# Kernel optimization log

Hardware: AMD Instinct MI355X
Metric: run time of the kernel (lower is better)

The kernel has to match this reference:

```python
import jax, jax.numpy as jnp
import numpy as np
from jax import lax

NPOINT, RADIUS, NSAMPLE, EPS = 2048, 0.1, 32, 1e-5


def setup_inputs() -> dict:
    key = jax.random.key(0)
    ks = jax.random.split(key, 8)
    B, N, D, CIN, COUT, DEPTH = 4, 8192, 29, 32, 64, 2
    return {
        "xyz": jax.random.uniform(ks[0], (B, 3, N), jnp.float32),
        "points": jax.random.normal(ks[1], (B, D, N), jnp.float32),
        "proj_w": jax.random.normal(ks[2], (COUT, CIN), jnp.float32) * 0.05,
        "proj_g": jnp.ones((COUT,), jnp.float32),
        "proj_b": jnp.zeros((COUT,), jnp.float32),
        "w1": jax.random.normal(ks[3], (DEPTH, COUT, COUT), jnp.float32) * 0.05,
        "g1": jnp.ones((DEPTH, COUT), jnp.float32),
        "b1": jnp.zeros((DEPTH, COUT), jnp.float32),
        "w2": jax.random.normal(ks[4], (DEPTH, COUT, COUT), jnp.float32) * 0.05,
        "g2": jnp.ones((DEPTH, COUT), jnp.float32),
        "b2": jnp.zeros((DEPTH, COUT), jnp.float32),
    }


def fps(xyz, npoint):
    # xyz: [B,N,3] -> idx [B,npoint]; deterministic start at index 0
    B, N, _ = xyz.shape
    def body(carry, _):
        dist, far = carry  # [B,N], [B]
        centroid = jnp.take_along_axis(xyz, far[:, None, None], axis=1)  # [B,1,3]
        d = jnp.sum((xyz - centroid) ** 2, -1)
        dist = jnp.minimum(dist, d)
        return (dist, jnp.argmax(dist, -1).astype(jnp.int32)), far
    init = (jnp.full((B, N), 1e10, xyz.dtype), jnp.zeros((B,), jnp.int32))
    _, idx = lax.scan(body, init, None, length=npoint)
    return jnp.transpose(idx)  # [B,npoint]


def ball_query(radius, nsample, xyz, new_xyz):
    # matches torch query_ball_point: invalid -> N, sort, take first nsample, backfill
    N = xyz.shape[1]
    sqr = (jnp.sum(new_xyz ** 2, -1)[:, :, None]
           + jnp.sum(xyz ** 2, -1)[:, None, :]
           - 2.0 * jnp.einsum("bsc,bnc->bsn", new_xyz, xyz))  # [B,S,N]
    cand = jnp.where(sqr <= radius * radius, jnp.arange(N, dtype=jnp.int32), jnp.int32(N))
    neg, _ = lax.top_k(-cand, nsample)
    idx = -neg  # nsample smallest indices, ascending
    first = idx[:, :, :1]
    return jnp.where(idx == N, first, idx)  # [B,S,K]


def gather_nb(p, idx):
    # p [B,N,C], idx [B,S,K] -> [B,S,K,C]
    return jax.vmap(lambda pb, ib: pb[ib])(p, idx)


def _conv(x, w):
    # 1x1 conv: w [O,C], x [B,C,K,S]
    return jnp.einsum("oc,bcks->boks", w, x)


def _bn(x, g, b):
    # training-mode BatchNorm2d over (B,K,S) per channel
    m = jnp.mean(x, (0, 2, 3), keepdims=True)
    v = jnp.var(x, (0, 2, 3), keepdims=True)
    return g[None, :, None, None] * (x - m) * lax.rsqrt(v + EPS) + b[None, :, None, None]


def reference(xyz, points, proj_w, proj_g, proj_b, w1, g1, b1, w2, g2, b2):
    xyz_t = jnp.transpose(xyz, (0, 2, 1))      # [B,N,3]
    pts_t = jnp.transpose(points, (0, 2, 1))   # [B,N,D]
    fidx = fps(xyz_t, NPOINT)                  # [B,S]
    new_xyz = jnp.take_along_axis(xyz_t, fidx[:, :, None], axis=1)  # [B,S,3]
    idx = ball_query(RADIUS, NSAMPLE, xyz_t, new_xyz)               # [B,S,K]
    grouped_xyz = gather_nb(xyz_t, idx) - new_xyz[:, :, None, :]    # [B,S,K,3]
    grouped_pts = gather_nb(pts_t, idx)                             # [B,S,K,D]
    new_points = jnp.concatenate([grouped_xyz, grouped_pts], -1)    # [B,S,K,3+D]
    x = jnp.transpose(new_points, (0, 3, 2, 1))                     # [B,C,K,S]
    x = jax.nn.relu(_bn(_conv(x, proj_w), proj_g, proj_b))
    for d in range(w1.shape[0]):
        idn = x
        x = jax.nn.relu(_bn(_conv(x, w1[d]), g1[d], b1[d]))
        x = _bn(_conv(x, w2[d]), g2[d], b2[d])
        x = jax.nn.relu(x + idn)
    feat = jnp.max(x, axis=2)                  # [B,Cout,S]
    return jnp.transpose(new_xyz, (0, 2, 1)), feat
```

## Files before the change

### kernel.cpp

```cpp
#include <hip/hip_runtime.h>
#include <cstdint>
#include <cstddef>

#define NPTS    8192
#define NPT     2048
#define KNB     32
#define NB      4
#define DPTS    29
#define CINP    32
#define CO      64
#define KS      (KNB*NPT)
#define TELEM   ((size_t)NB*CO*KS)
#define MCNT    262144.0f
#define BNEPS   1e-5f
#define FTHR    512
#define FWAVES  (FTHR/64)
#define FPT     16

#define FPS_STEP(J)                                                      \
    {                                                                    \
        float dx = __fsub_rn(px##J, cx);                                 \
        float dy = __fsub_rn(py##J, cy);                                 \
        float dz = __fsub_rn(pz##J, cz);                                 \
        float dd = __fadd_rn(__fadd_rn(__fmul_rn(dx, dx),                \
                                       __fmul_rn(dy, dy)),               \
                             __fmul_rn(dz, dz));                         \
        float nd = fminf(d##J, dd);                                      \
        d##J = nd;                                                       \
        bool gt = nd > tb;                                               \
        tb = gt ? nd : tb;                                               \
        jj = gt ? J : jj;                                                \
    }

static __device__ __forceinline__ unsigned long long umax64(unsigned long long a,
                                                            unsigned long long b) {
    return a > b ? a : b;
}

__global__ __launch_bounds__(FTHR) void fps_kernel(const float* __restrict__ xyz,
                                                   float* __restrict__ out0) {
    const int b = blockIdx.x;
    const int t = threadIdx.x;
    const int lane = t & 63;
    const int wid  = t >> 6;
    const float* xb = xyz + (size_t)b * 3 * NPTS;
    const int base = t * FPT;

    extern __shared__ float smem[];
    float* sx = smem;
    float* sy = sx + NPTS;
    float* sz = sy + NPTS;
    unsigned long long* skey = (unsigned long long*)(sz + NPTS);

    float px0,px1,px2,px3,px4,px5,px6,px7,px8,px9,px10,px11,px12,px13,px14,px15;
    float py0,py1,py2,py3,py4,py5,py6,py7,py8,py9,py10,py11,py12,py13,py14,py15;
    float pz0,pz1,pz2,pz3,pz4,pz5,pz6,pz7,pz8,pz9,pz10,pz11,pz12,pz13,pz14,pz15;
    float d0,d1,d2,d3,d4,d5,d6,d7,d8,d9,d10,d11,d12,d13,d14,d15;
    {
        const float4* x4 = (const float4*)(xb + base);
        const float4* y4 = (const float4*)(xb + NPTS + base);
        const float4* z4 = (const float4*)(xb + 2 * NPTS + base);
        float4* lx4 = (float4*)(sx + base);
        float4* ly4 = (float4*)(sy + base);
        float4* lz4 = (float4*)(sz + base);
        float4 v;
        v = x4[0]; lx4[0] = v; px0 =v.x; px1 =v.y; px2 =v.z; px3 =v.w;
        v = x4[1]; lx4[1] = v; px4 =v.x; px5 =v.y; px6 =v.z; px7 =v.w;
        v = x4[2]; lx4[2] = v; px8 =v.x; px9 =v.y; px10=v.z; px11=v.w;
        v = x4[3]; lx4[3] = v; px12=v.x; px13=v.y; px14=v.z; px15=v.w;
        v = y4[0]; ly4[0] = v; py0 =v.x; py1 =v.y; py2 =v.z; py3 =v.w;
        v = y4[1]; ly4[1] = v; py4 =v.x; py5 =v.y; py6 =v.z; py7 =v.w;
        v = y4[2]; ly4[2] = v; py8 =v.x; py9 =v.y; py10=v.z; py11=v.w;
        v = y4[3]; ly4[3] = v; py12=v.x; py13=v.y; py14=v.z; py15=v.w;
        v = z4[0]; lz4[0] = v; pz0 =v.x; pz1 =v.y; pz2 =v.z; pz3 =v.w;
        v = z4[1]; lz4[1] = v; pz4 =v.x; pz5 =v.y; pz6 =v.z; pz7 =v.w;
        v = z4[2]; lz4[2] = v; pz8 =v.x; pz9 =v.y; pz10=v.z; pz11=v.w;
        v = z4[3]; lz4[3] = v; pz12=v.x; pz13=v.y; pz14=v.z; pz15=v.w;
        d0=d1=d2=d3=d4=d5=d6=d7=d8=d9=d10=d11=d12=d13=d14=d15 = 1e10f;
    }

    float cx = xb[0], cy = xb[NPTS], cz = xb[2 * NPTS];
    float* ob = out0 + (size_t)b * 3 * NPT;
    if (t == 0) { ob[0] = cx; ob[NPT] = cy; ob[2 * NPT] = cz; }

    for (int i = 1; i < NPT; ++i) {
        float tb = -1.0f;
        int   jj = 0;
        FPS_STEP(0)  FPS_STEP(1)  FPS_STEP(2)  FPS_STEP(3)
        FPS_STEP(4)  FPS_STEP(5)  FPS_STEP(6)  FPS_STEP(7)
        FPS_STEP(8)  FPS_STEP(9)  FPS_STEP(10) FPS_STEP(11)
        FPS_STEP(12) FPS_STEP(13) FPS_STEP(14) FPS_STEP(15)
        const int gidx = base + jj;

        float wm = tb;
#pragma unroll
        for (int o = 32; o > 0; o >>= 1) wm = fmaxf(wm, __shfl_xor(wm, o, 64));
        unsigned long long eq = __ballot(tb == wm);
        const int lwin = __ffsll((long long)eq) - 1;
        const int wgid = __shfl(gidx, lwin, 64);

        const int par = i & 1;
        if (lane == 0)
            skey[par * FWAVES + wid] =
                (((unsigned long long)__float_as_uint(wm)) << 32) |
                (unsigned int)(~(unsigned int)wgid);
        __syncthreads();

        const ulonglong2* sk2 = (const ulonglong2*)(skey + par * FWAVES);
        ulonglong2 k01 = sk2[0], k23 = sk2[1], k45 = sk2[2], k67 = sk2[3];
        unsigned long long ka = umax64(k01.x, k01.y);
        unsigned long long kb = umax64(k23.x, k23.y);
        unsigned long long kc = umax64(k45.x, k45.y);
        unsigned long long kd = umax64(k67.x, k67.y);
        unsigned long long kbest = umax64(umax64(ka, kb), umax64(kc, kd));
        const int widx = (int)(~(unsigned int)kbest);

        cx = sx[widx]; cy = sy[widx]; cz = sz[widx];
        if (t == 0) { ob[i] = cx; ob[NPT + i] = cy; ob[2 * NPT + i] = cz; }
    }
}

__global__ __launch_bounds__(256) void ballq_kernel(const float* __restrict__ xyz,
                                                    const float* __restrict__ out0,
                                                    int* __restrict__ idx) {
    const int gw   = (blockIdx.x * 256 + threadIdx.x) >> 6;
    const int lane = threadIdx.x & 63;
    const int b  = gw >> 11;
    const int si = gw & 2047;
    const float* xb = xyz + (size_t)b * 3 * NPTS;

    const float cx = out0[b * 3 * NPT + si];
    const float cy = out0[b * 3 * NPT + NPT + si];
    const float cz = out0[b * 3 * NPT + 2*NPT + si];
    const float csum = __fadd_rn(__fadd_rn(__fmul_rn(cx, cx), __fmul_rn(cy, cy)),
                                 __fmul_rn(cz, cz));
    const float R2 = (float)(0.1 * 0.1);

    __shared__ int buf[4][KNB];
    int* mybuf = buf[threadIdx.x >> 6];

    int cnt = 0;
    for (int n0 = 0; n0 < NPTS && cnt < KNB; n0 += 64) {
        const int i = n0 + lane;
        float pxv = xb[i], pyv = xb[NPTS + i], pzv = xb[2 * NPTS + i];
        float ps = __fadd_rn(__fadd_rn(__fmul_rn(pxv, pxv), __fmul_rn(pyv, pyv)),
                             __fmul_rn(pzv, pzv));
        float dot = __fmaf_rn(pzv, cz, __fmaf_rn(pyv, cy, __fmul_rn(pxv, cx)));
        float sqr = __fsub_rn(__fadd_rn(csum, ps), __fadd_rn(dot, dot));
        bool hit = (sqr <= R2);
        unsigned long long m = __ballot(hit);
        int pos = cnt + __popcll(m & ((1ull << lane) - 1ull));
        if (hit && pos < KNB) mybuf[pos] = i;
        cnt += __popcll(m);
    }
    __syncthreads();
    int c = cnt < KNB ? cnt : KNB;
    int first = (cnt > 0) ? mybuf[0] : 0;
    if (lane < KNB) {
        int v = (lane < c) ? mybuf[lane] : first;
        idx[((size_t)gw << 5) + lane] = v;
    }
}

__global__ __launch_bounds__(256) void proj_kernel(const float* __restrict__ xyz,
                                                   const float* __restrict__ points,
                                                   const float* __restrict__ out0,
                                                   const int* __restrict__ idx,
                                                   const float* __restrict__ W,
                                                   float* __restrict__ out,
                                                   float* __restrict__ stats) {
    const int p = blockIdx.x * 256 + threadIdx.x;
    const int b = p >> 16;
    const int q = p & 65535;
    const int k = q >> 11;
    const int s = q & 2047;
    const int tid = threadIdx.x;

    __shared__ float ssum[CO], ssq[CO];
    if (tid < CO) { ssum[tid] = 0.f; ssq[tid] = 0.f; }
    __syncthreads();

    const int j = idx[((size_t)(b * NPT + s) << 5) + k];
    const float* xb = xyz + (size_t)b * 3 * NPTS;
    float a[CINP];
    a[0] = xb[j]            - out0[b * 3 * NPT + s];
    a[1] = xb[NPTS + j]     - out0[b * 3 * NPT + NPT + s];
    a[2] = xb[2*NPTS + j]   - out0[b * 3 * NPT + 2*NPT + s];
    const float* pb = points + (size_t)b * DPTS * NPTS;
#pragma unroll
    for (int c = 0; c < DPTS; ++c) a[3 + c] = pb[c * NPTS + j];

    const size_t obase = (size_t)b * CO * KS + q;
    for (int o = 0; o < CO; ++o) {
        float acc = 0.f;
#pragma unroll
        for (int c = 0; c < CINP; ++c) acc = __fmaf_rn(W[o * CINP + c], a[c], acc);
        out[obase + (size_t)o * KS] = acc;
        float s1 = acc, s2 = acc * acc;
#pragma unroll
        for (int off = 32; off > 0; off >>= 1) {
            s1 += __shfl_xor(s1, off, 64);
            s2 += __shfl_xor(s2, off, 64);
        }
        if ((tid & 63) == 0) { atomicAdd(&ssum[o], s1); atomicAdd(&ssq[o], s2); }
    }
    __syncthreads();
    if (tid < CO) {
        atomicAdd(&stats[tid], ssum[tid]);
        atomicAdd(&stats[CO + tid], ssq[tid]);
    }
}

template <bool HAS_IDN, bool WRITE_ACT>
__global__ __launch_bounds__(256) void conv_bn_kernel(const float* in,
                                                      const float* idn,
                                                      const float* __restrict__ stats_in,
                                                      const float* __restrict__ gamma,
                                                      const float* __restrict__ beta,
                                                      const float* __restrict__ W,
                                                      float* act_out,
                                                      float* out,
                                                      float* __restrict__ stats_out) {
    const int p = blockIdx.x * 256 + threadIdx.x;
    const int b = p >> 16;
    const int q = p & 65535;
    const int tid = threadIdx.x;

    __shared__ float ssc[CO], ssh[CO], ssum[CO], ssq[CO];
    if (tid < CO) {
        const float Minv = 1.0f / MCNT;
        float m = stats_in[tid] * Minv;
        float v = stats_in[CO + tid] * Minv - m * m;
        float scl = gamma[tid] * rsqrtf(v + BNEPS);
        ssc[tid] = scl;
        ssh[tid] = beta[tid] - m * scl;
        ssum[tid] = 0.f; ssq[tid] = 0.f;
    }
    __syncthreads();

    const size_t base = (size_t)b * CO * KS + q;
    float a[CO];
#pragma unroll
    for (int c = 0; c < CO; ++c) {
        float v = __fmaf_rn(ssc[c], in[base + (size_t)c * KS], ssh[c]);
        if (HAS_IDN) v += idn[base + (size_t)c * KS];
        v = fmaxf(v, 0.0f);
        a[c] = v;
        if (WRITE_ACT) act_out[base + (size_t)c * KS] = v;
    }
    for (int o = 0; o < CO; ++o) {
        float acc = 0.f;
#pragma unroll
        for (int c = 0; c < CO; ++c) acc = __fmaf_rn(W[o * CO + c], a[c], acc);
        out[base + (size_t)o * KS] = acc;
        float s1 = acc, s2 = acc * acc;
#pragma unroll
        for (int off = 32; off > 0; off >>= 1) {
            s1 += __shfl_xor(s1, off, 64);
            s2 += __shfl_xor(s2, off, 64);
        }
        if ((tid & 63) == 0) { atomicAdd(&ssum[o], s1); atomicAdd(&ssq[o], s2); }
    }
    __syncthreads();
    if (tid < CO) {
        atomicAdd(&stats_out[tid], ssum[tid]);
        atomicAdd(&stats_out[CO + tid], ssq[tid]);
    }
}

__global__ __launch_bounds__(256) void final_kernel(const float* __restrict__ y2,
                                                    const float* __restrict__ idn,
                                                    const float* __restrict__ stats,
                                                    const float* __restrict__ gamma,
                                                    const float* __restrict__ beta,
                                                    float* __restrict__ feat) {
    const int p = blockIdx.x * 256 + threadIdx.x;
    const int s = p & 2047;
    const int o = (p >> 11) & 63;
    const int b = p >> 17;
    const float Minv = 1.0f / MCNT;
    float m = stats[o] * Minv;
    float v = stats[CO + o] * Minv - m * m;
    float scl = gamma[o] * rsqrtf(v + BNEPS);
    float sh  = beta[o] - m * scl;
    const size_t base = (size_t)b * CO * KS + (size_t)o * KS + s;
    float mx = -1e30f;
#pragma unroll
    for (int k = 0; k < KNB; ++k) {
        float val = __fmaf_rn(scl, y2[base + (size_t)k * NPT], sh) + idn[base + (size_t)k * NPT];
        val = fmaxf(val, 0.0f);
        mx = fmaxf(mx, val);
    }
    feat[p] = mx;
}

__global__ void zero_kernel(float* p, int n) {
    int i = blockIdx.x * blockDim.x + threadIdx.x;
    if (i < n) p[i] = 0.f;
}

extern "C" void kernel_launch(void* const* d_in, const int* in_sizes, int n_in,
                              void* d_out, int out_size, void* d_ws, size_t ws_size,
                              hipStream_t stream) {
    (void)in_sizes; (void)n_in; (void)out_size; (void)ws_size;
    const float* xyz    = (const float*)d_in[0];
    const float* points = (const float*)d_in[1];
    const float* proj_w = (const float*)d_in[2];
    const float* proj_g = (const float*)d_in[3];
    const float* proj_b = (const float*)d_in[4];
    const float* w1     = (const float*)d_in[5];
    const float* g1     = (const float*)d_in[6];
    const float* b1     = (const float*)d_in[7];
    const float* w2     = (const float*)d_in[8];
    const float* g2     = (const float*)d_in[9];
    const float* b2     = (const float*)d_in[10];

    float* out0 = (float*)d_out;
    float* feat = (float*)d_out + NB * 3 * NPT;

    float* stats = (float*)d_ws;
    int*   idx   = (int*)((float*)d_ws + 1024);
    float* A     = (float*)(idx + NB * NPT * KNB);
    float* B     = A + TELEM;

    const size_t fps_lds = (size_t)(3 * NPTS) * sizeof(float)
                         + 2 * FWAVES * sizeof(unsigned long long);

    hipLaunchKernelGGL(zero_kernel, dim3(3), dim3(256), 0, stream, stats, 5 * 2 * CO);
    hipLaunchKernelGGL(fps_kernel, dim3(NB), dim3(FTHR), fps_lds, stream, xyz, out0);
    hipLaunchKernelGGL(ballq_kernel, dim3(2048), dim3(256), 0, stream, xyz, out0, idx);
    hipLaunchKernelGGL(proj_kernel, dim3(1024), dim3(256), 0, stream,
                       xyz, points, out0, idx, proj_w, A, stats);
    hipLaunchKernelGGL((conv_bn_kernel<false, true>), dim3(1024), dim3(256), 0, stream,
                       A, (const float*)nullptr, stats, proj_g, proj_b, w1,
                       B, A, stats + 128);
    hipLaunchKernelGGL((conv_bn_kernel<false, false>), dim3(1024), dim3(256), 0, stream,
                       A, (const float*)nullptr, stats + 128, g1, b1, w2,
                       (float*)nullptr, A, stats + 256);
    hipLaunchKernelGGL((conv_bn_kernel<true, true>), dim3(1024), dim3(256), 0, stream,
                       A, B, stats + 256, g2, b2, w1 + CO * CO,
                       B, A, stats + 384);
    hipLaunchKernelGGL((conv_bn_kernel<false, false>), dim3(1024), dim3(256), 0, stream,
                       A, (const float*)nullptr, stats + 384, g1 + CO, b1 + CO, w2 + CO * CO,
                       (float*)nullptr, A, stats + 512);
    hipLaunchKernelGGL(final_kernel, dim3(2048), dim3(256), 0, stream,
                       A, B, stats + 512, g2 + CO, b2 + CO, feat);
}
```

Before: 2.759 ms.

## Use packed FP32 math and DPP wave reduction in FPS inner loop

The per-point distance update in the farthest-point-sampling loop now uses v_pk_add/v_pk_mul inline asm, so two points are processed per instruction. The running argmax is replaced by a plain max followed by an equality scan to recover the first index. The wave-level max reduction moves from shuffle-xor to DPP row_shr/row_bcast plus readlane, and the winner broadcast uses readlane instead of shfl. The goal is to shorten the serial 2048-iteration critical path. The risks are the fixed s_nop hazard padding, the equality-based index recovery, and DPP bcast semantics on gfx950.

```diff
diff --git a/kernel.cpp b/kernel.cpp
--- a/kernel.cpp
+++ b/kernel.cpp
@@ -17,19 +17,22 @@
 #define FWAVES  (FTHR/64)
 #define FPT     16
 
-#define FPS_STEP(J)                                                      \
-    {                                                                    \
-        float dx = __fsub_rn(px##J, cx);                                 \
-        float dy = __fsub_rn(py##J, cy);                                 \
-        float dz = __fsub_rn(pz##J, cz);                                 \
-        float dd = __fadd_rn(__fadd_rn(__fmul_rn(dx, dx),                \
-                                       __fmul_rn(dy, dy)),               \
-                             __fmul_rn(dz, dz));                         \
-        float nd = fminf(d##J, dd);                                      \
-        d##J = nd;                                                       \
-        bool gt = nd > tb;                                               \
-        tb = gt ? nd : tb;                                               \
-        jj = gt ? J : jj;                                                \
+typedef float v2f __attribute__((ext_vector_type(2)));
+
+#define FPS_PAIR(P, A, B)                                                     \
+    {                                                                         \
+        v2f dx_, dy_, dz_, xx_, yy_, zz_, ss_, dd_;                           \
+        asm("v_pk_add_f32 %0, %1, %2" : "=v"(dx_) : "v"(px##P), "v"(ncx));    \
+        asm("v_pk_add_f32 %0, %1, %2" : "=v"(dy_) : "v"(py##P), "v"(ncy));    \
+        asm("v_pk_add_f32 %0, %1, %2" : "=v"(dz_) : "v"(pz##P), "v"(ncz));    \
+        asm("v_pk_mul_f32 %0, %1, %1" : "=v"(xx_) : "v"(dx_));                \
+        asm("v_pk_mul_f32 %0, %1, %1" : "=v"(yy_) : "v"(dy_));                \
+        asm("v_pk_mul_f32 %0, %1, %1" : "=v"(zz_) : "v"(dz_));                \
+        asm("v_pk_add_f32 %0, %1, %2" : "=v"(ss_) : "v"(xx_), "v"(yy_));      \
+        asm("v_pk_add_f32 %0, %1, %2" : "=v"(dd_) : "v"(ss_), "v"(zz_));      \
+        float ndA = fminf(d##A, dd_.x);  d##A = ndA;                          \
+        float ndB = fminf(d##B, dd_.y);  d##B = ndB;                          \
+        tb = fmaxf(fmaxf(tb, ndA), ndB);                                      \
     }
 
 static __device__ __forceinline__ unsigned long long umax64(unsigned long long a,
@@ -52,9 +55,9 @@
     float* sz = sy + NPTS;
     unsigned long long* skey = (unsigned long long*)(sz + NPTS);
 
-    float px0,px1,px2,px3,px4,px5,px6,px7,px8,px9,px10,px11,px12,px13,px14,px15;
-    float py0,py1,py2,py3,py4,py5,py6,py7,py8,py9,py10,py11,py12,py13,py14,py15;
-    float pz0,pz1,pz2,pz3,pz4,pz5,pz6,pz7,pz8,pz9,pz10,pz11,pz12,pz13,pz14,pz15;
+    v2f px0,px1,px2,px3,px4,px5,px6,px7;
+    v2f py0,py1,py2,py3,py4,py5,py6,py7;
+    v2f pz0,pz1,pz2,pz3,pz4,pz5,pz6,pz7;
     float d0,d1,d2,d3,d4,d5,d6,d7,d8,d9,d10,d11,d12,d13,d14,d15;
     {
         const float4* x4 = (const float4*)(xb + base);
@@ -64,18 +67,18 @@
         float4* ly4 = (float4*)(sy + base);
         float4* lz4 = (float4*)(sz + base);
         float4 v;
-        v = x4[0]; lx4[0] = v; px0 =v.x; px1 =v.y; px2 =v.z; px3 =v.w;
-        v = x4[1]; lx4[1] = v; px4 =v.x; px5 =v.y; px6 =v.z; px7 =v.w;
-        v = x4[2]; lx4[2] = v; px8 =v.x; px9 =v.y; px10=v.z; px11=v.w;
-        v = x4[3]; lx4[3] = v; px12=v.x; px13=v.y; px14=v.z; px15=v.w;
-        v = y4[0]; ly4[0] = v; py0 =v.x; py1 =v.y; py2 =v.z; py3 =v.w;
-        v = y4[1]; ly4[1] = v; py4 =v.x; py5 =v.y; py6 =v.z; py7 =v.w;
-        v = y4[2]; ly4[2] = v; py8 =v.x; py9 =v.y; py10=v.z; py11=v.w;
-        v = y4[3]; ly4[3] = v; py12=v.x; py13=v.y; py14=v.z; py15=v.w;
-        v = z4[0]; lz4[0] = v; pz0 =v.x; pz1 =v.y; pz2 =v.z; pz3 =v.w;
-        v = z4[1]; lz4[1] = v; pz4 =v.x; pz5 =v.y; pz6 =v.z; pz7 =v.w;
-        v = z4[2]; lz4[2] = v; pz8 =v.x; pz9 =v.y; pz10=v.z; pz11=v.w;
-        v = z4[3]; lz4[3] = v; pz12=v.x; pz13=v.y; pz14=v.z; pz15=v.w;
+        v = x4[0]; lx4[0] = v; px0 = (v2f){v.x, v.y}; px1 = (v2f){v.z, v.w};
+        v = x4[1]; lx4[1] = v; px2 = (v2f){v.x, v.y}; px3 = (v2f){v.z, v.w};
+        v = x4[2]; lx4[2] = v; px4 = (v2f){v.x, v.y}; px5 = (v2f){v.z, v.w};
+        v = x4[3]; lx4[3] = v; px6 = (v2f){v.x, v.y}; px7 = (v2f){v.z, v.w};
+        v = y4[0]; ly4[0] = v; py0 = (v2f){v.x, v.y}; py1 = (v2f){v.z, v.w};
+        v = y4[1]; ly4[1] = v; py2 = (v2f){v.x, v.y}; py3 = (v2f){v.z, v.w};
+        v = y4[2]; ly4[2] = v; py4 = (v2f){v.x, v.y}; py5 = (v2f){v.z, v.w};
+        v = y4[3]; ly4[3] = v; py6 = (v2f){v.x, v.y}; py7 = (v2f){v.z, v.w};
+        v = z4[0]; lz4[0] = v; pz0 = (v2f){v.x, v.y}; pz1 = (v2f){v.z, v.w};
+        v = z4[1]; lz4[1] = v; pz2 = (v2f){v.x, v.y}; pz3 = (v2f){v.z, v.w};
+        v = z4[2]; lz4[2] = v; pz4 = (v2f){v.x, v.y}; pz5 = (v2f){v.z, v.w};
+        v = z4[3]; lz4[3] = v; pz6 = (v2f){v.x, v.y}; pz7 = (v2f){v.z, v.w};
         d0=d1=d2=d3=d4=d5=d6=d7=d8=d9=d10=d11=d12=d13=d14=d15 = 1e10f;
     }
 
@@ -84,20 +87,56 @@
     if (t == 0) { ob[0] = cx; ob[NPT] = cy; ob[2 * NPT] = cz; }
 
     for (int i = 1; i < NPT; ++i) {
+        const v2f ncx = (v2f){-cx, -cx};
+        const v2f ncy = (v2f){-cy, -cy};
+        const v2f ncz = (v2f){-cz, -cz};
         float tb = -1.0f;
-        int   jj = 0;
-        FPS_STEP(0)  FPS_STEP(1)  FPS_STEP(2)  FPS_STEP(3)
-        FPS_STEP(4)  FPS_STEP(5)  FPS_STEP(6)  FPS_STEP(7)
-        FPS_STEP(8)  FPS_STEP(9)  FPS_STEP(10) FPS_STEP(11)
-        FPS_STEP(12) FPS_STEP(13) FPS_STEP(14) FPS_STEP(15)
+        FPS_PAIR(0, 0, 1)   FPS_PAIR(1, 2, 3)
+        FPS_PAIR(2, 4, 5)   FPS_PAIR(3, 6, 7)
+        FPS_PAIR(4, 8, 9)   FPS_PAIR(5, 10, 11)
+        FPS_PAIR(6, 12, 13) FPS_PAIR(7, 14, 15)
+
+        int jj = 0;
+        jj = (d15 == tb) ? 15 : jj;
+        jj = (d14 == tb) ? 14 : jj;
+        jj = (d13 == tb) ? 13 : jj;
+        jj = (d12 == tb) ? 12 : jj;
+        jj = (d11 == tb) ? 11 : jj;
+        jj = (d10 == tb) ? 10 : jj;
+        jj = (d9  == tb) ?  9 : jj;
+        jj = (d8  == tb) ?  8 : jj;
+        jj = (d7  == tb) ?  7 : jj;
+        jj = (d6  == tb) ?  6 : jj;
+        jj = (d5  == tb) ?  5 : jj;
+        jj = (d4  == tb) ?  4 : jj;
+        jj = (d3  == tb) ?  3 : jj;
+        jj = (d2  == tb) ?  2 : jj;
+        jj = (d1  == tb) ?  1 : jj;
+        jj = (d0  == tb) ?  0 : jj;
         const int gidx = base + jj;
 
-        float wm = tb;
-#pragma unroll
-        for (int o = 32; o > 0; o >>= 1) wm = fmaxf(wm, __shfl_xor(wm, o, 64));
+        float r = tb;
+        asm volatile(
+            "s_nop 1\n\t"
+            "v_max_f32 %0, %0, %0 row_shr:1\n\t"
+            "s_nop 1\n\t"
+            "v_max_f32 %0, %0, %0 row_shr:2\n\t"
+            "s_nop 1\n\t"
+            "v_max_f32 %0, %0, %0 row_shr:4\n\t"
+            "s_nop 1\n\t"
+            "v_max_f32 %0, %0, %0 row_shr:8\n\t"
+            "s_nop 1\n\t"
+            "v_max_f32 %0, %0, %0 row_bcast:15 row_mask:0xa\n\t"
+            "s_nop 1\n\t"
+            "v_max_f32 %0, %0, %0 row_bcast:31 row_mask:0xc\n\t"
+            "s_nop 1"
+            : "+v"(r));
+        const float wm = __uint_as_float(
+            (unsigned int)__builtin_amdgcn_readlane((int)__float_as_uint(r), 63));
+
         unsigned long long eq = __ballot(tb == wm);
         const int lwin = __ffsll((long long)eq) - 1;
-        const int wgid = __shfl(gidx, lwin, 64);
+        const int wgid = __builtin_amdgcn_readlane(gidx, lwin);
 
         const int par = i & 1;
         if (lane == 0)
```

New measurement: 2.439 ms. -11.6%, faster.
